# Optimization experiments

Hardware: AMD Instinct MI355X
Metric: run time of the kernel (lower is better)

Reference implementation:

```python
import jax, jax.numpy as jnp
import numpy as np

D_MODEL = 1024
NUM_HEADS = 16
D_K = D_MODEL // NUM_HEADS
ROPE_THETA = 10000.0


def setup_inputs() -> dict:
    key = jax.random.key(0)
    kx, kq, kk, kv, ko = jax.random.split(key, 5)
    B, S = 4, 2048
    std = (2.0 / (D_MODEL + D_MODEL)) ** 0.5
    def w(k):
        return jax.random.truncated_normal(k, -3.0, 3.0, (D_MODEL, D_MODEL), jnp.float32) * std
    return {
        "x": jax.random.normal(kx, (B, S, D_MODEL), jnp.float32),
        "Wq": w(kq), "Wk": w(kk), "Wv": w(kv), "Wo": w(ko),
    }


def _apply_rope(t):
    # t: [B, H, S, d_k]
    S, dk = t.shape[-2], t.shape[-1]
    inv_freq = 1.0 / (ROPE_THETA ** (jnp.arange(0, dk, 2) / dk))  # [dk/2]
    angles = jnp.outer(jnp.arange(S), inv_freq)                    # [S, dk/2]
    cos = jnp.repeat(jnp.cos(angles), 2, axis=-1).astype(t.dtype)  # [S, dk]
    sin = jnp.repeat(jnp.sin(angles), 2, axis=-1).astype(t.dtype)
    t_even = t[..., 0::2]
    t_odd = t[..., 1::2]
    t_rot = jnp.stack([-t_odd, t_even], axis=-1).reshape(t.shape)
    return t * cos + t_rot * sin


def reference(x, Wq, Wk, Wv, Wo):
    B, S, D = x.shape
    H, dk = NUM_HEADS, D_K
    q = jnp.einsum("bsi,io->bso", x, Wq).reshape(B, S, H, dk).swapaxes(1, 2)
    k = jnp.einsum("bsi,io->bso", x, Wk).reshape(B, S, H, dk).swapaxes(1, 2)
    v = jnp.einsum("bsi,io->bso", x, Wv).reshape(B, S, H, dk).swapaxes(1, 2)
    q = _apply_rope(q)
    k = _apply_rope(k)
    scores = jnp.einsum("bhqd,bhkd->bhqk", q, k) / (dk ** 0.5)  # [B,H,S,S]
    causal = jnp.tril(jnp.ones((S, S), dtype=bool))
    scores = jnp.where(causal, scores, -jnp.inf)
    attn = jax.nn.softmax(scores, axis=-1)
    out = jnp.einsum("bhqk,bhkd->bhqd", attn, v)  # [B,H,S,dk]
    out = out.swapaxes(1, 2).reshape(B, S, D)
    return jnp.einsum("bsi,io->bso", out, Wo)
```

## Files before the change

kernel.cpp:

```cpp
#include <hip/hip_runtime.h>
#include <hip/hip_bf16.h>

#define SEQ   2048
#define NB    4
#define NH    16
#define DK    64
#define DM    1024
#define MROWS (NB * SEQ)

typedef __bf16 bf16_t;
typedef __bf16 bf16x8 __attribute__((ext_vector_type(8)));
typedef __bf16 bf16x4 __attribute__((ext_vector_type(4)));
typedef float  f32x4  __attribute__((ext_vector_type(4)));

#define MFMA16(a, b, c) __builtin_amdgcn_mfma_f32_16x16x32_bf16((a), (b), (c), 0, 0, 0)

__device__ __forceinline__ void gl2lds16(const bf16_t* g, bf16_t* l) {
    __builtin_amdgcn_global_load_lds(
        (const __attribute__((address_space(1))) unsigned int*)g,
        (__attribute__((address_space(3))) unsigned int*)l, 16, 0, 0);
}

__global__ __launch_bounds__(256) void cvt_kernel(
    const float* __restrict__ in, bf16_t* __restrict__ out, int n)
{
    int i = (blockIdx.x * 256 + threadIdx.x) * 4;
    if (i + 3 < n) {
        const float4 v = *(const float4*)(in + i);
        bf16x4 o;
        o[0] = (bf16_t)v.x; o[1] = (bf16_t)v.y;
        o[2] = (bf16_t)v.z; o[3] = (bf16_t)v.w;
        *(bf16x4*)(out + i) = o;
    }
}

__global__ __launch_bounds__(256) void wtr_kernel(
    const float* __restrict__ W, bf16_t* __restrict__ Wt)
{
    __shared__ float T[32][33];
    const int tk0 = (blockIdx.x >> 5) << 5;
    const int tn0 = (blockIdx.x & 31) << 5;
    const int r = threadIdx.x >> 5, c = threadIdx.x & 31;
#pragma unroll
    for (int i = 0; i < 4; ++i)
        T[r + i * 8][c] = W[(size_t)(tk0 + r + i * 8) * DM + tn0 + c];
    __syncthreads();
#pragma unroll
    for (int i = 0; i < 4; ++i)
        Wt[(size_t)(tn0 + r + i * 8) * DM + tk0 + c] = (bf16_t)T[c][r + i * 8];
}

__global__ void rope_table_kernel(float2* __restrict__ tab) {
    int idx = blockIdx.x * 256 + threadIdx.x;
    if (idx >= SEQ * 32) return;
    int s = idx >> 5, i = idx & 31;
    float freq = powf(10000.0f, -(float)i / 32.0f);
    float a = (float)s * freq;
    tab[idx] = make_float2(cosf(a), sinf(a));
}

template<bool TR>
__device__ __forceinline__ void kloop128(
    const bf16_t* __restrict__ Xp, const bf16_t* __restrict__ Wp,
    bf16_t* As, bf16_t* Bs, int tid, f32x4 (&acc)[4][4], int kiters)
{
    const int lane = tid & 63;
    const int wave = tid >> 6;
    const int wm = wave & 1, wn = wave >> 1;
    const int l = lane & 15, quad = lane >> 4;
    const int rl = lane & 15;
    const int kf = (lane >> 4) << 3;
    const int gA = wave * 2;

    const bf16_t* xa0 = Xp + (size_t)(gA * 16 + rl) * DM + kf;
    const bf16_t* xa1 = Xp + (size_t)((gA + 1) * 16 + rl) * DM + kf;
    const bf16_t* wb0 = Wp + (size_t)(gA * 16 + rl) * DM + kf;
    const bf16_t* wb1 = Wp + (size_t)((gA + 1) * 16 + rl) * DM + kf;

    gl2lds16(xa0, As + gA * 512);
    gl2lds16(xa1, As + (gA + 1) * 512);
    gl2lds16(wb0, Bs + gA * 512);
    gl2lds16(wb1, Bs + (gA + 1) * 512);

    for (int k = 0; k < kiters; ++k) {
        const int cur = k & 1;
        __syncthreads();
        if (k + 1 < kiters) {
            const int nxt = cur ^ 1;
            const int ko = (k + 1) * 32;
            gl2lds16(xa0 + ko, As + nxt * 4096 + gA * 512);
            gl2lds16(xa1 + ko, As + nxt * 4096 + (gA + 1) * 512);
            gl2lds16(wb0 + ko, Bs + nxt * 4096 + gA * 512);
            gl2lds16(wb1 + ko, Bs + nxt * 4096 + (gA + 1) * 512);
        }
        const bf16_t* ab = As + cur * 4096;
        const bf16_t* bb = Bs + cur * 4096;
        bf16x8 af[4], bw[4];
#pragma unroll
        for (int a = 0; a < 4; ++a) {
            af[a] = *(const bf16x8*)(ab + (wm * 4 + a) * 512 + (quad * 16 + l) * 8);
            bw[a] = *(const bf16x8*)(bb + (wn * 4 + a) * 512 + (quad * 16 + l) * 8);
        }
#pragma unroll
        for (int a = 0; a < 4; ++a)
#pragma unroll
            for (int b = 0; b < 4; ++b)
                acc[a][b] = TR ? MFMA16(bw[b], af[a], acc[a][b])
                               : MFMA16(af[a], bw[b], acc[a][b]);
    }
}

__global__ __launch_bounds__(256) void gemm_qkv_kernel(
    const bf16_t* __restrict__ X, const bf16_t* __restrict__ Wt,
    bf16_t* __restrict__ Qt, bf16_t* __restrict__ Kt, bf16_t* __restrict__ Vtr,
    const float2* __restrict__ rope)
{
    __shared__ __align__(16) bf16_t As[2 * 128 * 32];
    __shared__ __align__(16) bf16_t Bs[2 * 128 * 32];

    const int tid  = threadIdx.x;
    const int lane = tid & 63;
    const int wave = tid >> 6;
    const int wm   = wave & 1, wn = wave >> 1;
    const int l    = lane & 15;
    const int quad = lane >> 4;

    const int m0 = (blockIdx.x / 24) << 7;
    const int n0 = (blockIdx.x % 24) << 7;
    const bool tr = (n0 >= 2 * DM);

    f32x4 acc[4][4] = {};
    if (tr) kloop128<true >(X + (size_t)m0 * DM, Wt + (size_t)n0 * DM, As, Bs, tid, acc, DM / 32);
    else    kloop128<false>(X + (size_t)m0 * DM, Wt + (size_t)n0 * DM, As, Bs, tid, acc, DM / 32);

#pragma unroll
    for (int a = 0; a < 4; ++a)
#pragma unroll
        for (int b = 0; b < 4; ++b)
#pragma unroll
            for (int r = 0; r < 4; ++r) {
                float v = acc[a][b][r];
                if (tr) {
                    const int n = n0 + wn * 64 + b * 16 + quad * 4 + r;
                    const int m = m0 + wm * 64 + a * 16 + l;
                    const int bi = m >> 11, s = m & (SEQ - 1);
                    const int col = n & (DM - 1);
                    const int h = col >> 6, d = col & (DK - 1);
                    Vtr[(((size_t)(bi * NH + h)) * DK + d) * SEQ + s] = (bf16_t)v;
                } else {
                    const int m  = m0 + wm * 64 + a * 16 + quad * 4 + r;
                    const int nn = n0 + wn * 64 + b * 16 + l;
                    const int bi = m >> 11, s = m & (SEQ - 1);
                    const int col = nn & (DM - 1);
                    const int h = col >> 6, d = col & (DK - 1);
                    float pv = __shfl_xor(v, 1);
                    float2 cs = rope[s * 32 + (d >> 1)];
                    float res = (d & 1) ? (v * cs.x + pv * cs.y)
                                        : (v * cs.x - pv * cs.y);
                    bf16_t* dst = (nn < DM) ? Qt : Kt;
                    if (nn < DM) res *= 0.125f;
                    dst[(((size_t)(bi * NH + h)) * SEQ + s) * DK + d] = (bf16_t)res;
                }
            }
}

__global__ __launch_bounds__(256) void gemm_out_kernel(
    const bf16_t* __restrict__ X, const bf16_t* __restrict__ Wt,
    float* __restrict__ out)
{
    __shared__ __align__(16) bf16_t As[2 * 128 * 32];
    __shared__ __align__(16) bf16_t Bs[2 * 128 * 32];

    const int tid  = threadIdx.x;
    const int lane = tid & 63;
    const int wave = tid >> 6;
    const int wm   = wave & 1, wn = wave >> 1;
    const int l    = lane & 15;
    const int quad = lane >> 4;

    const int m0 = (blockIdx.x >> 3) << 7;
    const int n0 = (blockIdx.x & 7) << 7;

    f32x4 acc[4][4] = {};
    kloop128<false>(X + (size_t)m0 * DM, Wt + (size_t)n0 * DM, As, Bs, tid, acc, DM / 32);

#pragma unroll
    for (int a = 0; a < 4; ++a)
#pragma unroll
        for (int b = 0; b < 4; ++b)
#pragma unroll
            for (int r = 0; r < 4; ++r) {
                const int m  = m0 + wm * 64 + a * 16 + quad * 4 + r;
                const int nn = n0 + wn * 64 + b * 16 + l;
                out[(size_t)m * DM + nn] = acc[a][b][r];
            }
}

#define KLD 72

__global__ __launch_bounds__(256) void attn_kernel(
    const bf16_t* __restrict__ Q, const bf16_t* __restrict__ K,
    const bf16_t* __restrict__ Vt, bf16_t* __restrict__ O)
{
    __shared__ __align__(16) bf16_t Kl[64 * KLD];
    __shared__ __align__(16) bf16_t Vl[64 * KLD];
    __shared__ __align__(16) bf16_t Pl[4][32 * KLD];

    const int bh   = blockIdx.y;
    const int tid  = threadIdx.x;
    const int wave = tid >> 6;
    const int lane = tid & 63;
    const int l    = lane & 15;
    const int quad = lane >> 4;
    const int srow = tid >> 3;
    const int sch  = (tid & 7) << 3;

    bf16_t* Pw = Pl[wave];
    const bf16_t* Qb = Q  + (size_t)bh * SEQ * DK;
    const bf16_t* Kb = K  + (size_t)bh * SEQ * DK;
    const bf16_t* Vb = Vt + (size_t)bh * DK * SEQ;
    const int b = bh >> 4, h = bh & 15;

    for (int ph = 0; ph < 2; ++ph) {
        const int qblk = ph ? (15 - (int)blockIdx.x) : (int)blockIdx.x;
        const int q0w  = qblk * 128 + wave * 32;
        const int nch  = 2 * (qblk + 1);

        bf16x8 qb[2][2];
#pragma unroll
        for (int u = 0; u < 2; ++u) {
            qb[u][0] = *(const bf16x8*)(Qb + (size_t)(q0w + u * 16 + l) * DK + quad * 8);
            qb[u][1] = *(const bf16x8*)(Qb + (size_t)(q0w + u * 16 + l) * DK + 32 + quad * 8);
        }

        float m_run[2] = {-3e38f, -3e38f};
        float l_run[2] = {0.f, 0.f};
        f32x4 o[4][2] = {};

        bf16x8 pk0 = *(const bf16x8*)(Kb + (size_t)srow * DK + sch);
        bf16x8 pk1 = *(const bf16x8*)(Kb + (size_t)(32 + srow) * DK + sch);
        bf16x8 pv0 = *(const bf16x8*)(Vb + (size_t)srow * SEQ + sch);
        bf16x8 pv1 = *(const bf16x8*)(Vb + (size_t)(32 + srow) * SEQ + sch);

        for (int i = 0; i < nch; ++i) {
            const int c = i * 64;
            __syncthreads();
            *(bf16x8*)(Kl + srow * KLD + sch)        = pk0;
            *(bf16x8*)(Kl + (32 + srow) * KLD + sch) = pk1;
            *(bf16x8*)(Vl + srow * KLD + sch)        = pv0;
            *(bf16x8*)(Vl + (32 + srow) * KLD + sch) = pv1;
            __syncthreads();
            if (i + 1 < nch) {
                const int cn = c + 64;
                pk0 = *(const bf16x8*)(Kb + (size_t)(cn + srow) * DK + sch);
                pk1 = *(const bf16x8*)(Kb + (size_t)(cn + 32 + srow) * DK + sch);
                pv0 = *(const bf16x8*)(Vb + (size_t)srow * SEQ + cn + sch);
                pv1 = *(const bf16x8*)(Vb + (size_t)(32 + srow) * SEQ + cn + sch);
            }
            if (c > q0w + 31) continue;

            f32x4 st[4][2] = {};
#pragma unroll
            for (int t = 0; t < 4; ++t) {
                const bf16x8 k0 = *(const bf16x8*)(Kl + (t * 16 + l) * KLD + quad * 8);
                const bf16x8 k1 = *(const bf16x8*)(Kl + (t * 16 + l) * KLD + 32 + quad * 8);
                st[t][0] = MFMA16(k0, qb[0][0], st[t][0]);
                st[t][0] = MFMA16(k1, qb[0][1], st[t][0]);
                st[t][1] = MFMA16(k0, qb[1][0], st[t][1]);
                st[t][1] = MFMA16(k1, qb[1][1], st[t][1]);
            }
            if (c + 63 > q0w) {
#pragma unroll
                for (int u = 0; u < 2; ++u) {
                    const int thr = q0w + u * 16 + l - c - quad * 4;
#pragma unroll
                    for (int t = 0; t < 4; ++t)
#pragma unroll
                        for (int r = 0; r < 4; ++r)
                            if (t * 16 + r > thr) st[t][u][r] = -3e38f;
                }
            }
#pragma unroll
            for (int u = 0; u < 2; ++u) {
                float cmax = -3e38f;
#pragma unroll
                for (int t = 0; t < 4; ++t)
#pragma unroll
                    for (int r = 0; r < 4; ++r)
                        cmax = fmaxf(cmax, st[t][u][r]);
                cmax = fmaxf(cmax, __shfl_xor(cmax, 16));
                cmax = fmaxf(cmax, __shfl_xor(cmax, 32));
                const float mnew  = fmaxf(m_run[u], cmax);
                const float alpha = __expf(m_run[u] - mnew);
                m_run[u] = mnew;
                float csum = 0.f;
#pragma unroll
                for (int t = 0; t < 4; ++t)
#pragma unroll
                    for (int r = 0; r < 4; ++r) {
                        st[t][u][r] = __expf(st[t][u][r] - mnew);
                        csum += st[t][u][r];
                    }
                csum += __shfl_xor(csum, 16);
                csum += __shfl_xor(csum, 32);
                l_run[u] = l_run[u] * alpha + csum;
#pragma unroll
                for (int n = 0; n < 4; ++n)
#pragma unroll
                    for (int r = 0; r < 4; ++r)
                        o[n][u][r] *= alpha;
#pragma unroll
                for (int t = 0; t < 4; ++t) {
                    bf16x4 pk;
                    pk[0] = (bf16_t)st[t][u][0]; pk[1] = (bf16_t)st[t][u][1];
                    pk[2] = (bf16_t)st[t][u][2]; pk[3] = (bf16_t)st[t][u][3];
                    *(bf16x4*)(Pw + (u * 16 + l) * KLD + t * 16 + quad * 4) = pk;
                }
            }
            const bf16x8 pb00 = *(const bf16x8*)(Pw + l * KLD + quad * 8);
            const bf16x8 pb01 = *(const bf16x8*)(Pw + l * KLD + 32 + quad * 8);
            const bf16x8 pb10 = *(const bf16x8*)(Pw + (16 + l) * KLD + quad * 8);
            const bf16x8 pb11 = *(const bf16x8*)(Pw + (16 + l) * KLD + 32 + quad * 8);
#pragma unroll
            for (int n = 0; n < 4; ++n) {
                const bf16x8 v0 = *(const bf16x8*)(Vl + (n * 16 + l) * KLD + quad * 8);
                const bf16x8 v1 = *(const bf16x8*)(Vl + (n * 16 + l) * KLD + 32 + quad * 8);
                o[n][0] = MFMA16(v0, pb00, o[n][0]);
                o[n][0] = MFMA16(v1, pb01, o[n][0]);
                o[n][1] = MFMA16(v0, pb10, o[n][1]);
                o[n][1] = MFMA16(v1, pb11, o[n][1]);
            }
        }

#pragma unroll
        for (int u = 0; u < 2; ++u) {
            const float inv = 1.0f / l_run[u];
#pragma unroll
            for (int n = 0; n < 4; ++n) {
                bf16x4 ov;
                ov[0] = (bf16_t)(o[n][u][0] * inv); ov[1] = (bf16_t)(o[n][u][1] * inv);
                ov[2] = (bf16_t)(o[n][u][2] * inv); ov[3] = (bf16_t)(o[n][u][3] * inv);
                *(bf16x4*)(Pw + (u * 16 + l) * KLD + n * 16 + quad * 4) = ov;
            }
        }
        const int row  = lane >> 1;
        const int half = (lane & 1) * 32;
        const bf16x8 w0 = *(const bf16x8*)(Pw + row * KLD + half);
        const bf16x8 w1 = *(const bf16x8*)(Pw + row * KLD + half + 8);
        const bf16x8 w2 = *(const bf16x8*)(Pw + row * KLD + half + 16);
        const bf16x8 w3 = *(const bf16x8*)(Pw + row * KLD + half + 24);
        bf16_t* op = O + ((size_t)(b * SEQ + qblk * 128 + wave * 32 + row)) * DM
                       + h * DK + half;
        *(bf16x8*)(op)      = w0;
        *(bf16x8*)(op + 8)  = w1;
        *(bf16x8*)(op + 16) = w2;
        *(bf16x8*)(op + 24) = w3;
    }
}

extern "C" void kernel_launch(void* const* d_in, const int* in_sizes, int n_in,
                              void* d_out, int out_size, void* d_ws, size_t ws_size,
                              hipStream_t stream)
{
    const float* x  = (const float*)d_in[0];
    const float* Wq = (const float*)d_in[1];
    const float* Wk = (const float*)d_in[2];
    const float* Wv = (const float*)d_in[3];
    const float* Wo = (const float*)d_in[4];

    char* ws = (char*)d_ws;
    float2* rope = (float2*)ws;
    const size_t TEN = (size_t)MROWS * DM;
    const size_t WEL = (size_t)DM * DM;
    bf16_t* xb    = (bf16_t*)(ws + (1 << 19));
    bf16_t* Wqkvt = xb + TEN;
    bf16_t* Wot   = Wqkvt + 3 * WEL;
    bf16_t* Qt    = Wot + WEL;
    bf16_t* Kt    = Qt + TEN;
    bf16_t* Vt    = Kt + TEN;
    bf16_t* Ot    = Vt + TEN;

    rope_table_kernel<<<(SEQ * 32 + 255) / 256, 256, 0, stream>>>(rope);

    cvt_kernel<<<(int)(TEN / 4 / 256), 256, 0, stream>>>(x, xb, (int)TEN);
    wtr_kernel<<<1024, 256, 0, stream>>>(Wq, Wqkvt);
    wtr_kernel<<<1024, 256, 0, stream>>>(Wk, Wqkvt + WEL);
    wtr_kernel<<<1024, 256, 0, stream>>>(Wv, Wqkvt + 2 * WEL);
    wtr_kernel<<<1024, 256, 0, stream>>>(Wo, Wot);

    gemm_qkv_kernel<<<64 * 24, 256, 0, stream>>>(xb, Wqkvt, Qt, Kt, Vt, rope);

    attn_kernel<<<dim3(8, NB * NH), 256, 0, stream>>>(Qt, Kt, Vt, Ot);

    gemm_out_kernel<<<64 * 8, 256, 0, stream>>>(Ot, Wot, (float*)d_out);
}
```

Before: 341.3 us.

## Triple-buffer GEMM k-loop with direct-to-LDS prefetch two stages ahead

```diff
diff --git a/kernel.cpp b/kernel.cpp
--- a/kernel.cpp
+++ b/kernel.cpp
@@ -77,22 +77,27 @@
     const bf16_t* wb0 = Wp + (size_t)(gA * 16 + rl) * DM + kf;
     const bf16_t* wb1 = Wp + (size_t)((gA + 1) * 16 + rl) * DM + kf;
 
-    gl2lds16(xa0, As + gA * 512);
-    gl2lds16(xa1, As + (gA + 1) * 512);
-    gl2lds16(wb0, Bs + gA * 512);
-    gl2lds16(wb1, Bs + (gA + 1) * 512);
-
+#define STAGE(J, BUF) do {                                          \
+        const int _ko = (J) * 32;                                   \
+        gl2lds16(xa0 + _ko, As + (BUF) * 4096 + gA * 512);          \
+        gl2lds16(xa1 + _ko, As + (BUF) * 4096 + (gA + 1) * 512);    \
+        gl2lds16(wb0 + _ko, Bs + (BUF) * 4096 + gA * 512);          \
+        gl2lds16(wb1 + _ko, Bs + (BUF) * 4096 + (gA + 1) * 512);    \
+    } while (0)
+
+    STAGE(0, 0);
+    STAGE(1, 1);
+
+    int cur = 0;
+    int pre = 2;
     for (int k = 0; k < kiters; ++k) {
-        const int cur = k & 1;
-        __syncthreads();
         if (k + 1 < kiters) {
-            const int nxt = cur ^ 1;
-            const int ko = (k + 1) * 32;
-            gl2lds16(xa0 + ko, As + nxt * 4096 + gA * 512);
-            gl2lds16(xa1 + ko, As + nxt * 4096 + (gA + 1) * 512);
-            gl2lds16(wb0 + ko, Bs + nxt * 4096 + gA * 512);
-            gl2lds16(wb1 + ko, Bs + nxt * 4096 + (gA + 1) * 512);
+            asm volatile("s_waitcnt vmcnt(4)\n\ts_barrier" ::: "memory");
+        } else {
+            asm volatile("s_waitcnt vmcnt(0)\n\ts_barrier" ::: "memory");
         }
+        if (k + 2 < kiters) STAGE(k + 2, pre);
+
         const bf16_t* ab = As + cur * 4096;
         const bf16_t* bb = Bs + cur * 4096;
         bf16x8 af[4], bw[4];
@@ -107,7 +112,11 @@
             for (int b = 0; b < 4; ++b)
                 acc[a][b] = TR ? MFMA16(bw[b], af[a], acc[a][b])
                                : MFMA16(af[a], bw[b], acc[a][b]);
+
+        cur = (cur == 2) ? 0 : cur + 1;
+        pre = (pre == 2) ? 0 : pre + 1;
     }
+#undef STAGE
 }
 
 __global__ __launch_bounds__(256) void gemm_qkv_kernel(
@@ -115,8 +124,8 @@
     bf16_t* __restrict__ Qt, bf16_t* __restrict__ Kt, bf16_t* __restrict__ Vtr,
     const float2* __restrict__ rope)
 {
-    __shared__ __align__(16) bf16_t As[2 * 128 * 32];
-    __shared__ __align__(16) bf16_t Bs[2 * 128 * 32];
+    __shared__ __align__(16) bf16_t As[3 * 128 * 32];
+    __shared__ __align__(16) bf16_t Bs[3 * 128 * 32];
 
     const int tid  = threadIdx.x;
     const int lane = tid & 63;
@@ -168,8 +177,8 @@
     const bf16_t* __restrict__ X, const bf16_t* __restrict__ Wt,
     float* __restrict__ out)
 {
-    __shared__ __align__(16) bf16_t As[2 * 128 * 32];
-    __shared__ __align__(16) bf16_t Bs[2 * 128 * 32];
+    __shared__ __align__(16) bf16_t As[3 * 128 * 32];
+    __shared__ __align__(16) bf16_t Bs[3 * 128 * 32];
 
     const int tid  = threadIdx.x;
     const int lane = tid & 63;
```

Result: no change. 339.2 us (-0.6%).

## Rewrite GEMMs as 256x256 tiles with 8 waves, explicit pipelining, XCD-aware mapping

Applied to the files above, without the earlier changes.

```diff
diff --git a/kernel.cpp b/kernel.cpp
--- a/kernel.cpp
+++ b/kernel.cpp
@@ -59,97 +59,149 @@
     tab[idx] = make_float2(cosf(a), sinf(a));
 }
 
+#define SBAR()   asm volatile("s_barrier" ::: "memory")
+#define VMC(N)   asm volatile("s_waitcnt vmcnt(" #N ")" ::: "memory")
+
 template<bool TR>
-__device__ __forceinline__ void kloop128(
+__device__ __forceinline__ void kloop256(
     const bf16_t* __restrict__ Xp, const bf16_t* __restrict__ Wp,
-    bf16_t* As, bf16_t* Bs, int tid, f32x4 (&acc)[4][4], int kiters)
+    bf16_t* L, int tid, f32x4 (&acc)[8][4], int kt)
 {
     const int lane = tid & 63;
     const int wave = tid >> 6;
-    const int wm = wave & 1, wn = wave >> 1;
-    const int l = lane & 15, quad = lane >> 4;
-    const int rl = lane & 15;
-    const int kf = (lane >> 4) << 3;
-    const int gA = wave * 2;
-
-    const bf16_t* xa0 = Xp + (size_t)(gA * 16 + rl) * DM + kf;
-    const bf16_t* xa1 = Xp + (size_t)((gA + 1) * 16 + rl) * DM + kf;
-    const bf16_t* wb0 = Wp + (size_t)(gA * 16 + rl) * DM + kf;
-    const bf16_t* wb1 = Wp + (size_t)((gA + 1) * 16 + rl) * DM + kf;
-
-    gl2lds16(xa0, As + gA * 512);
-    gl2lds16(xa1, As + (gA + 1) * 512);
-    gl2lds16(wb0, Bs + gA * 512);
-    gl2lds16(wb1, Bs + (gA + 1) * 512);
-
-    for (int k = 0; k < kiters; ++k) {
-        const int cur = k & 1;
-        __syncthreads();
-        if (k + 1 < kiters) {
-            const int nxt = cur ^ 1;
-            const int ko = (k + 1) * 32;
-            gl2lds16(xa0 + ko, As + nxt * 4096 + gA * 512);
-            gl2lds16(xa1 + ko, As + nxt * 4096 + (gA + 1) * 512);
-            gl2lds16(wb0 + ko, Bs + nxt * 4096 + gA * 512);
-            gl2lds16(wb1 + ko, Bs + nxt * 4096 + (gA + 1) * 512);
+    const int wm   = wave & 1;
+    const int wn   = wave >> 1;
+    const int lrow = lane & 15;
+    const int lcol = (lane >> 4) << 3;
+
+    bf16_t* const As = L;
+    bf16_t* const Bs = L + 4 * 8192;
+
+    auto stA = [&](int t, int half) {
+        const bf16_t* g = Xp + (size_t)(half * 128 + wave * 16 + lrow) * DM + t * 64 + lcol;
+        bf16_t* s = As + ((t & 1) * 2 + half) * 8192 + wave * 1024;
+        gl2lds16(g,      s);
+        gl2lds16(g + 32, s + 512);
+    };
+    auto stB = [&](int t, int half) {
+        const bf16_t* g = Wp + (size_t)(half * 128 + wave * 16 + lrow) * DM + t * 64 + lcol;
+        bf16_t* s = Bs + ((t & 1) * 2 + half) * 8192 + wave * 1024;
+        gl2lds16(g,      s);
+        gl2lds16(g + 32, s + 512);
+    };
+
+    const bf16_t* const Aw = As + wm * 8192;
+    const bf16_t* const Bw = Bs + (wn >> 1) * 8192;
+    const int bgrp = (wn & 1) * 4;
+
+    stA(0, 0); stA(0, 1); stB(0, 0); stB(0, 1);
+    stB(1, 0); stB(1, 1);
+    VMC(4);
+    SBAR();
+
+    const int nit = kt >> 1;
+    for (int it = 0; it < nit; ++it) {
+        const int t = 2 * it;
+        const bool lst = (t + 2 >= kt);
+
+#pragma unroll
+        for (int par = 0; par < 2; ++par) {
+            bf16x8 bf[8];
+#pragma unroll
+            for (int q = 0; q < 4; ++q) {
+                const bf16_t* ap = Aw + par * 16384;
+                bf16x8 a00 = *(const bf16x8*)(ap + (q * 4 + 0) * 512 + lane * 8);
+                bf16x8 a01 = *(const bf16x8*)(ap + (q * 4 + 1) * 512 + lane * 8);
+                bf16x8 a10 = *(const bf16x8*)(ap + (q * 4 + 2) * 512 + lane * 8);
+                bf16x8 a11 = *(const bf16x8*)(ap + (q * 4 + 3) * 512 + lane * 8);
+                if (q == 0) {
+                    const bf16_t* bp = Bw + par * 16384;
+#pragma unroll
+                    for (int nf = 0; nf < 4; ++nf) {
+                        bf[nf * 2]     = *(const bf16x8*)(bp + ((bgrp + nf) * 2 + 0) * 512 + lane * 8);
+                        bf[nf * 2 + 1] = *(const bf16x8*)(bp + ((bgrp + nf) * 2 + 1) * 512 + lane * 8);
+                    }
+                }
+                if (par == 0) {
+                    if (q == 0) { stA(t + 1, 0); stA(t + 1, 1); }
+                    else if (q == 1) { if (!lst) stB(t + 2, 0); }
+                    else if (q == 2) { if (!lst) stB(t + 2, 1); }
+                } else {
+                    if (q == 0)      { if (!lst) stA(t + 2, 0); }
+                    else if (q == 1) { if (!lst) stA(t + 2, 1); }
+                    else if (q == 2) { if (!lst) stB(t + 3, 0); }
+                    else             { if (!lst) stB(t + 3, 1); }
+                }
+                SBAR();
+                __builtin_amdgcn_s_setprio(1);
+#pragma unroll
+                for (int nf = 0; nf < 4; ++nf) {
+                    if (TR) {
+                        acc[q * 2 + 0][nf] = MFMA16(bf[nf * 2],     a00, acc[q * 2 + 0][nf]);
+                        acc[q * 2 + 0][nf] = MFMA16(bf[nf * 2 + 1], a01, acc[q * 2 + 0][nf]);
+                        acc[q * 2 + 1][nf] = MFMA16(bf[nf * 2],     a10, acc[q * 2 + 1][nf]);
+                        acc[q * 2 + 1][nf] = MFMA16(bf[nf * 2 + 1], a11, acc[q * 2 + 1][nf]);
+                    } else {
+                        acc[q * 2 + 0][nf] = MFMA16(a00, bf[nf * 2],     acc[q * 2 + 0][nf]);
+                        acc[q * 2 + 0][nf] = MFMA16(a01, bf[nf * 2 + 1], acc[q * 2 + 0][nf]);
+                        acc[q * 2 + 1][nf] = MFMA16(a10, bf[nf * 2],     acc[q * 2 + 1][nf]);
+                        acc[q * 2 + 1][nf] = MFMA16(a11, bf[nf * 2 + 1], acc[q * 2 + 1][nf]);
+                    }
+                }
+                __builtin_amdgcn_s_setprio(0);
+                if (q == 3) {
+                    if (par == 0) { if (lst) { VMC(0); } else { VMC(4); } }
+                    else          { if (!lst) { VMC(4); } }
+                }
+                SBAR();
+            }
         }
-        const bf16_t* ab = As + cur * 4096;
-        const bf16_t* bb = Bs + cur * 4096;
-        bf16x8 af[4], bw[4];
-#pragma unroll
-        for (int a = 0; a < 4; ++a) {
-            af[a] = *(const bf16x8*)(ab + (wm * 4 + a) * 512 + (quad * 16 + l) * 8);
-            bw[a] = *(const bf16x8*)(bb + (wn * 4 + a) * 512 + (quad * 16 + l) * 8);
-        }
-#pragma unroll
-        for (int a = 0; a < 4; ++a)
-#pragma unroll
-            for (int b = 0; b < 4; ++b)
-                acc[a][b] = TR ? MFMA16(bw[b], af[a], acc[a][b])
-                               : MFMA16(af[a], bw[b], acc[a][b]);
     }
-}
-
-__global__ __launch_bounds__(256) void gemm_qkv_kernel(
+    VMC(0);
+}
+
+__global__ __launch_bounds__(512, 2) void gemm_qkv_kernel(
     const bf16_t* __restrict__ X, const bf16_t* __restrict__ Wt,
     bf16_t* __restrict__ Qt, bf16_t* __restrict__ Kt, bf16_t* __restrict__ Vtr,
     const float2* __restrict__ rope)
 {
-    __shared__ __align__(16) bf16_t As[2 * 128 * 32];
-    __shared__ __align__(16) bf16_t Bs[2 * 128 * 32];
-
-    const int tid  = threadIdx.x;
+    __shared__ __align__(16) bf16_t L[8 * 8192];
+
+    const int tid = threadIdx.x;
+    const int xcd = blockIdx.x & 7;
+    const int idx = blockIdx.x >> 3;
+    const int mt  = xcd * 4 + idx / 12;
+    const int nt  = idx % 12;
+    const int m0 = mt << 8, n0 = nt << 8;
+    const bool tr = (n0 >= 2 * DM);
+
+    f32x4 acc[8][4] = {};
+    if (tr) kloop256<true >(X + (size_t)m0 * DM, Wt + (size_t)n0 * DM, L, tid, acc, DM / 64);
+    else    kloop256<false>(X + (size_t)m0 * DM, Wt + (size_t)n0 * DM, L, tid, acc, DM / 64);
+
     const int lane = tid & 63;
     const int wave = tid >> 6;
     const int wm   = wave & 1, wn = wave >> 1;
     const int l    = lane & 15;
     const int quad = lane >> 4;
 
-    const int m0 = (blockIdx.x / 24) << 7;
-    const int n0 = (blockIdx.x % 24) << 7;
-    const bool tr = (n0 >= 2 * DM);
-
-    f32x4 acc[4][4] = {};
-    if (tr) kloop128<true >(X + (size_t)m0 * DM, Wt + (size_t)n0 * DM, As, Bs, tid, acc, DM / 32);
-    else    kloop128<false>(X + (size_t)m0 * DM, Wt + (size_t)n0 * DM, As, Bs, tid, acc, DM / 32);
-
-#pragma unroll
-    for (int a = 0; a < 4; ++a)
-#pragma unroll
-        for (int b = 0; b < 4; ++b)
+#pragma unroll
+    for (int mf = 0; mf < 8; ++mf)
+#pragma unroll
+        for (int nf = 0; nf < 4; ++nf)
 #pragma unroll
             for (int r = 0; r < 4; ++r) {
-                float v = acc[a][b][r];
+                float v = acc[mf][nf][r];
                 if (tr) {
-                    const int n = n0 + wn * 64 + b * 16 + quad * 4 + r;
-                    const int m = m0 + wm * 64 + a * 16 + l;
+                    const int n = n0 + wn * 64 + nf * 16 + quad * 4 + r;
+                    const int m = m0 + wm * 128 + mf * 16 + l;
                     const int bi = m >> 11, s = m & (SEQ - 1);
                     const int col = n & (DM - 1);
                     const int h = col >> 6, d = col & (DK - 1);
                     Vtr[(((size_t)(bi * NH + h)) * DK + d) * SEQ + s] = (bf16_t)v;
                 } else {
-                    const int m  = m0 + wm * 64 + a * 16 + quad * 4 + r;
-                    const int nn = n0 + wn * 64 + b * 16 + l;
+                    const int m  = m0 + wm * 128 + mf * 16 + quad * 4 + r;
+                    const int nn = n0 + wn * 64 + nf * 16 + l;
                     const int bi = m >> 11, s = m & (SEQ - 1);
                     const int col = nn & (DM - 1);
                     const int h = col >> 6, d = col & (DK - 1);
@@ -164,35 +216,37 @@
             }
 }
 
-__global__ __launch_bounds__(256) void gemm_out_kernel(
+__global__ __launch_bounds__(512, 2) void gemm_out_kernel(
     const bf16_t* __restrict__ X, const bf16_t* __restrict__ Wt,
     float* __restrict__ out)
 {
-    __shared__ __align__(16) bf16_t As[2 * 128 * 32];
-    __shared__ __align__(16) bf16_t Bs[2 * 128 * 32];
-
-    const int tid  = threadIdx.x;
+    __shared__ __align__(16) bf16_t L[8 * 8192];
+
+    const int tid = threadIdx.x;
+    const int xcd = blockIdx.x & 7;
+    const int idx = blockIdx.x >> 3;
+    const int mt  = xcd * 4 + idx / 4;
+    const int nt  = idx & 3;
+    const int m0 = mt << 8, n0 = nt << 8;
+
+    f32x4 acc[8][4] = {};
+    kloop256<false>(X + (size_t)m0 * DM, Wt + (size_t)n0 * DM, L, tid, acc, DM / 64);
+
     const int lane = tid & 63;
     const int wave = tid >> 6;
     const int wm   = wave & 1, wn = wave >> 1;
     const int l    = lane & 15;
     const int quad = lane >> 4;
 
-    const int m0 = (blockIdx.x >> 3) << 7;
-    const int n0 = (blockIdx.x & 7) << 7;
-
-    f32x4 acc[4][4] = {};
-    kloop128<false>(X + (size_t)m0 * DM, Wt + (size_t)n0 * DM, As, Bs, tid, acc, DM / 32);
-
-#pragma unroll
-    for (int a = 0; a < 4; ++a)
-#pragma unroll
-        for (int b = 0; b < 4; ++b)
+#pragma unroll
+    for (int mf = 0; mf < 8; ++mf)
+#pragma unroll
+        for (int nf = 0; nf < 4; ++nf)
 #pragma unroll
             for (int r = 0; r < 4; ++r) {
-                const int m  = m0 + wm * 64 + a * 16 + quad * 4 + r;
-                const int nn = n0 + wn * 64 + b * 16 + l;
-                out[(size_t)m * DM + nn] = acc[a][b][r];
+                const int m  = m0 + wm * 128 + mf * 16 + quad * 4 + r;
+                const int nn = n0 + wn * 64 + nf * 16 + l;
+                out[(size_t)m * DM + nn] = acc[mf][nf][r];
             }
 }
 
@@ -206,7 +260,8 @@
     __shared__ __align__(16) bf16_t Vl[64 * KLD];
     __shared__ __align__(16) bf16_t Pl[4][32 * KLD];
 
-    const int bh   = blockIdx.y;
+    const int bh   = blockIdx.x;
+    const int qx   = blockIdx.y;
     const int tid  = threadIdx.x;
     const int wave = tid >> 6;
     const int lane = tid & 63;
@@ -222,7 +277,7 @@
     const int b = bh >> 4, h = bh & 15;
 
     for (int ph = 0; ph < 2; ++ph) {
-        const int qblk = ph ? (15 - (int)blockIdx.x) : (int)blockIdx.x;
+        const int qblk = ph ? (15 - qx) : qx;
         const int q0w  = qblk * 128 + wave * 32;
         const int nch  = 2 * (qblk + 1);
 
@@ -388,9 +443,9 @@
     wtr_kernel<<<1024, 256, 0, stream>>>(Wv, Wqkvt + 2 * WEL);
     wtr_kernel<<<1024, 256, 0, stream>>>(Wo, Wot);
 
-    gemm_qkv_kernel<<<64 * 24, 256, 0, stream>>>(xb, Wqkvt, Qt, Kt, Vt, rope);
-
-    attn_kernel<<<dim3(8, NB * NH), 256, 0, stream>>>(Qt, Kt, Vt, Ot);
-
-    gemm_out_kernel<<<64 * 8, 256, 0, stream>>>(Ot, Wot, (float*)d_out);
-}
+    gemm_qkv_kernel<<<32 * 12, 512, 0, stream>>>(xb, Wqkvt, Qt, Kt, Vt, rope);
+
+    attn_kernel<<<dim3(NB * NH, 8), 256, 0, stream>>>(Qt, Kt, Vt, Ot);
+
+    gemm_out_kernel<<<32 * 4, 512, 0, stream>>>(Ot, Wot, (float*)d_out);
+}
```

Result: faster. 328.2 us (-3.8%).
